# Kernel tuning notes

Measured on AMD Instinct MI355X. Metric: run time of the kernel, lower is better.

The kernel has to match this reference:

```python
import jax, jax.numpy as jnp
import numpy as np

N = 100000   # nodes
E = 1600000  # edges
G = 256      # graphs
NF = 7       # node features
EF = 3       # edge features (in/out)
UD = 2       # global feature dim
H = 128      # hidden dim
NL = 2       # MetaLayers = n_layers - 1
DOUT = 1


def _lin_init(k, fan_in, fan_out):
    return jax.random.normal(k, (fan_in, fan_out), jnp.float32) / np.sqrt(fan_in)


def _mlp2(h, W1, b1, W2, b2):
    return jax.nn.relu(h @ W1 + b1) @ W2 + b2


def setup_inputs() -> dict:
    key = jax.random.key(0)
    ks = jax.random.split(key, 40)
    x = jax.random.normal(ks[0], (N, NF), jnp.float32)
    edge_index = jax.random.randint(ks[1], (2, E), 0, N, jnp.int64)
    edge_attr = jax.random.normal(ks[2], (E, EF), jnp.float32)
    u = jax.random.normal(ks[3], (G, UD), jnp.float32)
    batch = jnp.sort(jax.random.randint(ks[4], (N,), 0, G, jnp.int64))
    # stacked per-layer params (NL identical layers)
    e_in = 2 * NF + EF          # 17
    n_in = NF + 3 * EF + UD     # 18
    eW1 = jnp.stack([_lin_init(ks[5 + i], e_in, H) for i in range(NL)])
    eb1 = jnp.zeros((NL, H), jnp.float32)
    eW2 = jnp.stack([_lin_init(ks[7 + i], H, EF) for i in range(NL)])
    eb2 = jnp.zeros((NL, EF), jnp.float32)
    nW1 = jnp.stack([_lin_init(ks[9 + i], n_in, H) for i in range(NL)])
    nb1 = jnp.zeros((NL, H), jnp.float32)
    nW2 = jnp.stack([_lin_init(ks[11 + i], H, NF) for i in range(NL)])
    nb2 = jnp.zeros((NL, NF), jnp.float32)
    # output head: 3*node_out + global_in -> H -> H -> H -> dim_out
    oW1 = _lin_init(ks[20], 3 * NF + UD, H); ob1 = jnp.zeros((H,), jnp.float32)
    oW2 = _lin_init(ks[21], H, H); ob2 = jnp.zeros((H,), jnp.float32)
    oW3 = _lin_init(ks[22], H, H); ob3 = jnp.zeros((H,), jnp.float32)
    oW4 = _lin_init(ks[23], H, DOUT); ob4 = jnp.zeros((DOUT,), jnp.float32)
    return dict(x=x, edge_attr=edge_attr, u=u,
                eW1=eW1, eb1=eb1, eW2=eW2, eb2=eb2,
                nW1=nW1, nb1=nb1, nW2=nW2, nb2=nb2,
                oW1=oW1, ob1=ob1, oW2=oW2, ob2=ob2,
                oW3=oW3, ob3=ob3, oW4=oW4, ob4=ob4,
                edge_index=edge_index, batch=batch)


def _segment_reduce3(vals, seg, num):
    # add / max (empty -> 0, matching torch_scatter fill) / mean
    s = jax.ops.segment_sum(vals, seg, num_segments=num)
    cnt = jax.ops.segment_sum(jnp.ones((vals.shape[0], 1), vals.dtype), seg, num_segments=num)
    m = jax.ops.segment_max(vals, seg, num_segments=num)
    m = jnp.where(cnt > 0, m, jnp.zeros_like(m))
    mean = s / jnp.maximum(cnt, 1.0)
    return s, m, mean, cnt


def reference(x, edge_attr, u, eW1, eb1, eW2, eb2, nW1, nb1, nW2, nb2,
              oW1, ob1, oW2, ob2, oW3, ob3, oW4, ob4, edge_index, batch):
    row, col = edge_index[0], edge_index[1]
    for l in range(NL):
        # EdgeModel: gather src/dest node feats + edge feats -> MLP
        e_in = jnp.concatenate([x[row], x[col], edge_attr], axis=1)  # [E, 2*NF+EF]
        edge_attr = _mlp2(e_in, eW1[l], eb1[l], eW2[l], eb2[l])      # [E, EF]
        # NodeModel: three scatter reductions over incoming edges (col)
        s, m, mean, _ = _segment_reduce3(edge_attr, col, N)
        n_in = jnp.concatenate([x, s, m, mean, u[batch]], axis=1)    # [N, NF+3*EF+UD]
        x = _mlp2(n_in, nW1[l], nb1[l], nW2[l], nb2[l])              # [N, NF]
    # global pools per graph
    s, m, mean, _ = _segment_reduce3(x, batch, G)
    h = jnp.concatenate([s, mean, m, u], axis=1)                     # [G, 3*NF+UD]
    h = jax.nn.relu(h @ oW1 + ob1)
    h = jax.nn.relu(h @ oW2 + ob2)
    h = jax.nn.relu(h @ oW3 + ob3)
    return h @ oW4 + ob4                                             # [G, DOUT]
```

## Files before the change

### kernel.cpp

```cpp
#include <hip/hip_runtime.h>

#define NN 100000
#define NE 1600000
#define NG 256
#define NB 391
#define NBH 1024
#define CHUNK 1563
#define NBINS 1024
#define NBUCK 782

typedef __attribute__((ext_vector_type(8))) short short8v;
typedef __attribute__((ext_vector_type(4))) float float4v;

__device__ __forceinline__ unsigned short f2bf(float f) {
    unsigned u = __float_as_uint(f);
    return (unsigned short)((u + 0x7FFFu + ((u >> 16) & 1u)) >> 16);
}
__device__ __forceinline__ unsigned fenc(float f) {
    unsigned u = __float_as_uint(f);
    return (u & 0x80000000u) ? ~u : (u | 0x80000000u);
}
__device__ __forceinline__ float fdec(unsigned e) {
    return __uint_as_float((e & 0x80000000u) ? (e & 0x7FFFFFFFu) : ~e);
}

__global__ __launch_bounds__(256) void hist_kernel(
    const int* __restrict__ col, unsigned* __restrict__ ghist) {
    __shared__ unsigned h[NBINS];
    int b = blockIdx.x;
    for (int i = threadIdx.x; i < NBINS; i += 256) h[i] = 0;
    __syncthreads();
    int e0 = b * CHUNK;
    int e1 = e0 + CHUNK; if (e1 > NE) e1 = NE;
    for (int e = e0 + threadIdx.x; e < e1; e += 256)
        atomicAdd(&h[col[e] >> 7], 1u);
    __syncthreads();
    for (int i = threadIdx.x; i < NBINS; i += 256)
        ghist[(size_t)b * NBINS + i] = h[i];
}

__global__ __launch_bounds__(1024) void scanB_kernel(
    const unsigned* __restrict__ ghist, unsigned* __restrict__ goff,
    unsigned* __restrict__ total) {
    __shared__ unsigned a[NBH], bb[NBH];
    int bin = blockIdx.x, t = threadIdx.x;
    unsigned v = ghist[(size_t)t * NBINS + bin];
    a[t] = v;
    __syncthreads();
    unsigned* src = a; unsigned* dst = bb;
    for (int off = 1; off < NBH; off <<= 1) {
        unsigned x = src[t];
        if (t >= off) x += src[t - off];
        dst[t] = x;
        __syncthreads();
        unsigned* tmp = src; src = dst; dst = tmp;
    }
    goff[(size_t)t * NBINS + bin] = src[t] - v;
    if (t == NBH - 1) total[bin] = src[t];
}

__global__ __launch_bounds__(1024) void scanC_kernel(
    const unsigned* __restrict__ total, unsigned* __restrict__ binbase) {
    __shared__ unsigned a[NBINS], bb[NBINS];
    int t = threadIdx.x;
    unsigned v = total[t];
    a[t] = v;
    __syncthreads();
    unsigned* src = a; unsigned* dst = bb;
    for (int off = 1; off < NBINS; off <<= 1) {
        unsigned x = src[t];
        if (t >= off) x += src[t - off];
        dst[t] = x;
        __syncthreads();
        unsigned* tmp = src; src = dst; dst = tmp;
    }
    binbase[t] = src[t] - v;
    if (t == NBINS - 1) binbase[NBINS] = src[t];
}

__global__ __launch_bounds__(256) void scatterD_kernel(
    const int* __restrict__ row, const int* __restrict__ col,
    const float* __restrict__ ea,
    const unsigned* __restrict__ goff, const unsigned* __restrict__ binbase,
    int2* __restrict__ rc, float* __restrict__ eab) {
    __shared__ unsigned cur[NBINS];
    int b = blockIdx.x;
    for (int i = threadIdx.x; i < NBINS; i += 256) cur[i] = 0;
    __syncthreads();
    int e0 = b * CHUNK;
    int e1 = e0 + CHUNK; if (e1 > NE) e1 = NE;
    const unsigned* grow = goff + (size_t)b * NBINS;
    for (int e = e0 + threadIdx.x; e < e1; e += 256) {
        int c = col[e];
        int bin = c >> 7;
        unsigned l = atomicAdd(&cur[bin], 1u);
        unsigned slot = binbase[bin] + grow[bin] + l;
        rc[slot] = make_int2(row[e], c);
        eab[(size_t)slot * 3 + 0] = ea[(size_t)e * 3 + 0];
        eab[(size_t)slot * 3 + 1] = ea[(size_t)e * 3 + 1];
        eab[(size_t)slot * 3 + 2] = ea[(size_t)e * 3 + 2];
    }
}

__global__ __launch_bounds__(256) void gbound_kernel(
    const int* __restrict__ batch, int* __restrict__ gstart) {
    int n = blockIdx.x * 256 + threadIdx.x;
    if (n >= NN) return;
    int b = batch[n];
    int bp = (n == 0) ? -1 : batch[n - 1];
    for (int g = bp + 1; g <= b; ++g) gstart[g] = n;
    if (n == NN - 1) {
        for (int g = b + 1; g <= NG; ++g) gstart[g] = NN;
    }
}

__global__ __launch_bounds__(256) void prep_kernel(
    const float* __restrict__ eW1, const float* __restrict__ eb1, const float* __restrict__ eW2,
    const float* __restrict__ nW1, const float* __restrict__ nb1, const float* __restrict__ nW2,
    short* __restrict__ ewf, float* __restrict__ w2f, float* __restrict__ b1f,
    float* __restrict__ nwt)
{
    int t = blockIdx.x * 256 + threadIdx.x;
    const int EWF = 2 * 4096;
    const int W2F = 2 * 1536;
    const int B1F = 2 * 512;
    const int NWT = 2 * 128 * 28;
    if (t < EWF) {
        int layer = t >> 12, r = t & 4095;
        int tt = r >> 9, r2 = r & 511;
        int l = r2 >> 3, i = r2 & 7;
        int kk = ((l >> 4) << 3) + i;
        int n = tt * 16 + (l & 15);
        float v = (kk < 17) ? eW1[layer * 17 * 128 + kk * 128 + n] : 0.f;
        ewf[t] = (short)f2bf(v);
    } else if (t < EWF + W2F) {
        int q = t - EWF;
        int layer = q / 1536, r = q % 1536;
        int l = r / 24, r2 = r % 24;
        int tt = r2 / 3, c = r2 % 3;
        int k = tt * 16 + (l & 15);
        w2f[q] = eW2[layer * 384 + k * 3 + c];
    } else if (t < EWF + W2F + B1F) {
        int q = t - EWF - W2F;
        int layer = q / 512, r = q % 512;
        int l = r / 8, tt = r % 8;
        b1f[q] = eb1[layer * 128 + tt * 16 + (l & 15)];
    } else if (t < EWF + W2F + B1F + NWT) {
        int q = t - EWF - W2F - B1F;
        int l = q / (128 * 28), rest = q % (128 * 28), j = rest / 28, i = rest % 28;
        float v = 0.f;
        if (i < 18)       v = nW1[l * 18 * 128 + i * 128 + j];
        else if (i == 18) v = nb1[l * 128 + j];
        else if (i < 26)  v = nW2[l * 128 * 7 + j * 7 + (i - 19)];
        nwt[q] = v;
    }
}

__global__ __launch_bounds__(256) void edge_kernel(
    const float* __restrict__ x, float* eab,
    const int2* __restrict__ rc,
    const short* __restrict__ ewf, const float* __restrict__ w2f,
    const float* __restrict__ b1f, const float* __restrict__ b2)
{
    int lane = threadIdx.x & 63;
    int l15 = lane & 15, lg = lane >> 4;
    int wid = (blockIdx.x * 256 + threadIdx.x) >> 6;
    int nwaves = gridDim.x * 4;

    short8v B1[8];
    #pragma unroll
    for (int t = 0; t < 8; ++t)
        B1[t] = *(const short8v*)(ewf + (t * 64 + lane) * 8);
    float w2a[8], w2b[8], w2c[8], b1v[8];
    #pragma unroll
    for (int t = 0; t < 8; ++t) {
        w2a[t] = w2f[lane * 24 + t * 3 + 0];
        w2b[t] = w2f[lane * 24 + t * 3 + 1];
        w2c[t] = w2f[lane * 24 + t * 3 + 2];
        b1v[t] = b1f[lane * 8 + t];
    }
    float bb0 = b2[0], bb1 = b2[1], bb2 = b2[2];

    const int NT = NE / 16;
    for (int tile = wid; tile < NT; tile += nwaves) {
        int s = tile * 16 + l15;
        int2 p = rc[s];
        const float* xr = x + (size_t)p.x * 7;
        const float* xc = x + (size_t)p.y * 7;
        const float* ep = eab + (size_t)s * 3;

        float av0 = 0.f, av1 = 0.f, av2 = 0.f, av3 = 0.f,
              av4 = 0.f, av5 = 0.f, av6 = 0.f, av7 = 0.f;
        if (lg == 0) {
            av0 = xr[0]; av1 = xr[1]; av2 = xr[2]; av3 = xr[3];
            av4 = xr[4]; av5 = xr[5]; av6 = xr[6]; av7 = xc[0];
        } else if (lg == 1) {
            av0 = xc[1]; av1 = xc[2]; av2 = xc[3]; av3 = xc[4];
            av4 = xc[5]; av5 = xc[6]; av6 = ep[0]; av7 = ep[1];
        } else if (lg == 2) {
            av0 = ep[2];
        }

        short8v A;
        A[0] = (short)f2bf(av0); A[1] = (short)f2bf(av1);
        A[2] = (short)f2bf(av2); A[3] = (short)f2bf(av3);
        A[4] = (short)f2bf(av4); A[5] = (short)f2bf(av5);
        A[6] = (short)f2bf(av6); A[7] = (short)f2bf(av7);

        float4v Z = {0.f, 0.f, 0.f, 0.f};
        float4v C[8];
        #pragma unroll
        for (int t = 0; t < 8; ++t)
            C[t] = __builtin_amdgcn_mfma_f32_16x16x32_bf16(A, B1[t], Z, 0, 0, 0);

        float p00 = 0.f, p01 = 0.f, p02 = 0.f;
        float p10 = 0.f, p11 = 0.f, p12 = 0.f;
        float p20 = 0.f, p21 = 0.f, p22 = 0.f;
        float p30 = 0.f, p31 = 0.f, p32 = 0.f;
        #pragma unroll
        for (int t = 0; t < 8; ++t) {
            float h0 = fmaxf(C[t][0] + b1v[t], 0.f);
            float h1 = fmaxf(C[t][1] + b1v[t], 0.f);
            float h2 = fmaxf(C[t][2] + b1v[t], 0.f);
            float h3 = fmaxf(C[t][3] + b1v[t], 0.f);
            p00 += h0 * w2a[t]; p01 += h0 * w2b[t]; p02 += h0 * w2c[t];
            p10 += h1 * w2a[t]; p11 += h1 * w2b[t]; p12 += h1 * w2c[t];
            p20 += h2 * w2a[t]; p21 += h2 * w2b[t]; p22 += h2 * w2c[t];
            p30 += h3 * w2a[t]; p31 += h3 * w2b[t]; p32 += h3 * w2c[t];
        }
        #pragma unroll
        for (int m = 1; m < 16; m <<= 1) {
            p00 += __shfl_xor(p00, m, 16); p01 += __shfl_xor(p01, m, 16); p02 += __shfl_xor(p02, m, 16);
            p10 += __shfl_xor(p10, m, 16); p11 += __shfl_xor(p11, m, 16); p12 += __shfl_xor(p12, m, 16);
            p20 += __shfl_xor(p20, m, 16); p21 += __shfl_xor(p21, m, 16); p22 += __shfl_xor(p22, m, 16);
            p30 += __shfl_xor(p30, m, 16); p31 += __shfl_xor(p31, m, 16); p32 += __shfl_xor(p32, m, 16);
        }
        if (l15 < 4) {
            float o0 = (l15 == 0) ? p00 : (l15 == 1) ? p10 : (l15 == 2) ? p20 : p30;
            float o1 = (l15 == 0) ? p01 : (l15 == 1) ? p11 : (l15 == 2) ? p21 : p31;
            float o2 = (l15 == 0) ? p02 : (l15 == 1) ? p12 : (l15 == 2) ? p22 : p32;
            size_t off = (size_t)(tile * 16 + lg * 4 + l15) * 3;
            eab[off + 0] = o0 + bb0;
            eab[off + 1] = o1 + bb1;
            eab[off + 2] = o2 + bb2;
        }
    }
}

__global__ __launch_bounds__(256) void bucket_reduce_kernel(
    const float* __restrict__ eab, const int2* __restrict__ rc,
    const unsigned* __restrict__ binbase,
    const float* __restrict__ u, const int* __restrict__ batch,
    float* __restrict__ nred)
{
    __shared__ float s0[128], s1[128], s2[128];
    __shared__ unsigned m0[128], m1[128], m2[128], cc[128];
    int bin = blockIdx.x, t = threadIdx.x;
    if (t < 128) {
        s0[t] = 0.f; s1[t] = 0.f; s2[t] = 0.f;
        m0[t] = 0u; m1[t] = 0u; m2[t] = 0u; cc[t] = 0u;
    }
    __syncthreads();
    unsigned beg = binbase[bin], end = binbase[bin + 1];
    for (unsigned k = beg + t; k < end; k += 256) {
        int c = rc[k].y & 127;
        float v0 = eab[(size_t)k * 3 + 0];
        float v1 = eab[(size_t)k * 3 + 1];
        float v2 = eab[(size_t)k * 3 + 2];
        atomicAdd(&s0[c], v0); atomicAdd(&s1[c], v1); atomicAdd(&s2[c], v2);
        atomicMax(&m0[c], fenc(v0)); atomicMax(&m1[c], fenc(v1)); atomicMax(&m2[c], fenc(v2));
        atomicAdd(&cc[c], 1u);
    }
    __syncthreads();
    if (t < 128) {
        int n = (bin << 7) + t;
        if (n < NN) {
            unsigned c = cc[t];
            float cf = (float)c;
            float inv = 1.f / fmaxf(cf, 1.f);
            float S0 = s0[t], S1 = s1[t], S2 = s2[t];
            float M0 = c ? fdec(m0[t]) : 0.f;
            float M1 = c ? fdec(m1[t]) : 0.f;
            float M2 = c ? fdec(m2[t]) : 0.f;
            int b = batch[n];
            float* o = nred + (size_t)n * 12;
            o[0] = S0; o[1] = S1; o[2] = S2;
            o[3] = M0; o[4] = M1; o[5] = M2;
            o[6] = S0 * inv; o[7] = S1 * inv; o[8] = S2 * inv;
            o[9] = u[b * 2 + 0]; o[10] = u[b * 2 + 1];
        }
    }
}

#define NMLP_BLOCKS 1024
#define NMLP_WAVES (NMLP_BLOCKS * 4)
__global__ __launch_bounds__(256, 4) void nodemlp_kernel(
    const float* x_in, const float* __restrict__ nred,
    const float* __restrict__ wt, const float* __restrict__ b2,
    float* x_out)
{
    int lane = threadIdx.x & 63;
    int wid = (blockIdx.x * 256 + threadIdx.x) >> 6;

    const float* ra = wt + lane * 28;
    const float* rb = wt + (lane + 64) * 28;
    float a0 = ra[0], a1 = ra[1], a2 = ra[2], a3 = ra[3], a4 = ra[4], a5 = ra[5],
          a6 = ra[6], a7 = ra[7], a8 = ra[8], a9 = ra[9], a10 = ra[10], a11 = ra[11],
          a12 = ra[12], a13 = ra[13], a14 = ra[14], a15 = ra[15], a16 = ra[16], a17 = ra[17],
          ab = ra[18], p0 = ra[19], p1 = ra[20], p2 = ra[21], p3 = ra[22], p4 = ra[23],
          p5 = ra[24], p6 = ra[25];
    float b0 = rb[0], b1 = rb[1], b2_ = rb[2], b3 = rb[3], b4 = rb[4], b5 = rb[5],
          b6 = rb[6], b7 = rb[7], b8 = rb[8], b9 = rb[9], b10 = rb[10], b11 = rb[11],
          b12 = rb[12], b13 = rb[13], b14 = rb[14], b15 = rb[15], b16 = rb[16], b17 = rb[17],
          bb = rb[18], q0 = rb[19], q1 = rb[20], q2 = rb[21], q3 = rb[22], q4 = rb[23],
          q5 = rb[24], q6 = rb[25];

    asm volatile("" : "+v"(a0), "+v"(a1), "+v"(a2), "+v"(a3), "+v"(a4), "+v"(a5),
                      "+v"(a6), "+v"(a7), "+v"(a8), "+v"(a9), "+v"(a10), "+v"(a11),
                      "+v"(a12), "+v"(a13), "+v"(a14), "+v"(a15), "+v"(a16), "+v"(a17),
                      "+v"(ab), "+v"(p0), "+v"(p1), "+v"(p2), "+v"(p3), "+v"(p4),
                      "+v"(p5), "+v"(p6));
    asm volatile("" : "+v"(b0), "+v"(b1), "+v"(b2_), "+v"(b3), "+v"(b4), "+v"(b5),
                      "+v"(b6), "+v"(b7), "+v"(b8), "+v"(b9), "+v"(b10), "+v"(b11),
                      "+v"(b12), "+v"(b13), "+v"(b14), "+v"(b15), "+v"(b16), "+v"(b17),
                      "+v"(bb), "+v"(q0), "+v"(q1), "+v"(q2), "+v"(q3), "+v"(q4),
                      "+v"(q5), "+v"(q6));

    float B0 = b2[0], B1 = b2[1], B2 = b2[2], B3 = b2[3], B4 = b2[4], B5 = b2[5], B6 = b2[6];

    const int nper = (NN + NMLP_WAVES - 1) / NMLP_WAVES;
    int n0 = wid * nper;
    int n1 = n0 + nper; if (n1 > NN) n1 = NN;

    #pragma unroll 2
    for (int n = n0; n < n1; ++n) {
        int nu = __builtin_amdgcn_readfirstlane(n);
        const float* xp = x_in + (size_t)nu * 7;
        const float* rp = nred + (size_t)nu * 12;
        float i0 = xp[0], i1 = xp[1], i2 = xp[2], i3 = xp[3], i4 = xp[4], i5 = xp[5], i6 = xp[6];
        float s0 = rp[0], s1 = rp[1], s2 = rp[2];
        float m0 = rp[3], m1 = rp[4], m2 = rp[5];
        float e0 = rp[6], e1 = rp[7], e2 = rp[8];
        float u0 = rp[9], u1 = rp[10];

        float ha = ab, hb = bb;
        ha += i0 * a0;  hb += i0 * b0;
        ha += i1 * a1;  hb += i1 * b1;
        ha += i2 * a2;  hb += i2 * b2_;
        ha += i3 * a3;  hb += i3 * b3;
        ha += i4 * a4;  hb += i4 * b4;
        ha += i5 * a5;  hb += i5 * b5;
        ha += i6 * a6;  hb += i6 * b6;
        ha += s0 * a7;  hb += s0 * b7;
        ha += s1 * a8;  hb += s1 * b8;
        ha += s2 * a9;  hb += s2 * b9;
        ha += m0 * a10; hb += m0 * b10;
        ha += m1 * a11; hb += m1 * b11;
        ha += m2 * a12; hb += m2 * b12;
        ha += e0 * a13; hb += e0 * b13;
        ha += e1 * a14; hb += e1 * b14;
        ha += e2 * a15; hb += e2 * b15;
        ha += u0 * a16; hb += u0 * b16;
        ha += u1 * a17; hb += u1 * b17;
        ha = fmaxf(ha, 0.f); hb = fmaxf(hb, 0.f);

        float c0 = ha * p0 + hb * q0;
        float c1 = ha * p1 + hb * q1;
        float c2 = ha * p2 + hb * q2;
        float c3 = ha * p3 + hb * q3;
        float c4 = ha * p4 + hb * q4;
        float c5 = ha * p5 + hb * q5;
        float c6 = ha * p6 + hb * q6;
        #pragma unroll
        for (int msk = 1; msk < 64; msk <<= 1) {
            c0 += __shfl_xor(c0, msk);
            c1 += __shfl_xor(c1, msk);
            c2 += __shfl_xor(c2, msk);
            c3 += __shfl_xor(c3, msk);
            c4 += __shfl_xor(c4, msk);
            c5 += __shfl_xor(c5, msk);
            c6 += __shfl_xor(c6, msk);
        }
        float o = c0 + B0;
        if (lane == 1) o = c1 + B1;
        if (lane == 2) o = c2 + B2;
        if (lane == 3) o = c3 + B3;
        if (lane == 4) o = c4 + B4;
        if (lane == 5) o = c5 + B5;
        if (lane == 6) o = c6 + B6;
        if (lane < 7) x_out[(size_t)nu * 7 + lane] = o;
    }
}

__global__ __launch_bounds__(256) void pool_head_kernel(
    const float* __restrict__ x, const int* __restrict__ gstart,
    const float* __restrict__ u,
    const float* __restrict__ oW1, const float* __restrict__ ob1,
    const float* __restrict__ oW2, const float* __restrict__ ob2,
    const float* __restrict__ oW3, const float* __restrict__ ob3,
    const float* __restrict__ oW4, const float* __restrict__ ob4,
    float* __restrict__ out)
{
    int g = blockIdx.x, tid = threadIdx.x;
    int lane = tid & 63, wv = tid >> 6;
    int gs = gstart[g], ge = gstart[g + 1];

    float s0 = 0.f, s1 = 0.f, s2 = 0.f, s3 = 0.f, s4 = 0.f, s5 = 0.f, s6 = 0.f;
    float m0 = -__builtin_inff(), m1 = m0, m2 = m0, m3 = m0, m4 = m0, m5 = m0, m6 = m0;
    for (int n = gs + tid; n < ge; n += 256) {
        const float* xp = x + (size_t)n * 7;
        float v0 = xp[0], v1 = xp[1], v2 = xp[2], v3 = xp[3], v4 = xp[4], v5 = xp[5], v6 = xp[6];
        s0 += v0; s1 += v1; s2 += v2; s3 += v3; s4 += v4; s5 += v5; s6 += v6;
        m0 = fmaxf(m0, v0); m1 = fmaxf(m1, v1); m2 = fmaxf(m2, v2); m3 = fmaxf(m3, v3);
        m4 = fmaxf(m4, v4); m5 = fmaxf(m5, v5); m6 = fmaxf(m6, v6);
    }
    #pragma unroll
    for (int msk = 1; msk < 64; msk <<= 1) {
        s0 += __shfl_xor(s0, msk); s1 += __shfl_xor(s1, msk); s2 += __shfl_xor(s2, msk);
        s3 += __shfl_xor(s3, msk); s4 += __shfl_xor(s4, msk); s5 += __shfl_xor(s5, msk);
        s6 += __shfl_xor(s6, msk);
        m0 = fmaxf(m0, __shfl_xor(m0, msk)); m1 = fmaxf(m1, __shfl_xor(m1, msk));
        m2 = fmaxf(m2, __shfl_xor(m2, msk)); m3 = fmaxf(m3, __shfl_xor(m3, msk));
        m4 = fmaxf(m4, __shfl_xor(m4, msk)); m5 = fmaxf(m5, __shfl_xor(m5, msk));
        m6 = fmaxf(m6, __shfl_xor(m6, msk));
    }
    __shared__ float red[4][14];
    __shared__ float hin[23];
    __shared__ float ha[128];
    __shared__ float hbuf[128];
    if (lane == 0) {
        red[wv][0] = s0; red[wv][1] = s1; red[wv][2] = s2; red[wv][3] = s3;
        red[wv][4] = s4; red[wv][5] = s5; red[wv][6] = s6;
        red[wv][7] = m0; red[wv][8] = m1; red[wv][9] = m2; red[wv][10] = m3;
        red[wv][11] = m4; red[wv][12] = m5; red[wv][13] = m6;
    }
    __syncthreads();
    if (tid < 7) {
        float S = red[0][tid] + red[1][tid] + red[2][tid] + red[3][tid];
        float M = fmaxf(fmaxf(red[0][7 + tid], red[1][7 + tid]),
                        fmaxf(red[2][7 + tid], red[3][7 + tid]));
        float cntf = (float)(ge - gs);
        if (ge == gs) M = 0.f;
        hin[tid] = S;
        hin[7 + tid] = S / fmaxf(cntf, 1.f);
        hin[14 + tid] = M;
    }
    if (tid < 2) hin[21 + tid] = u[g * 2 + tid];
    __syncthreads();

    float h = 0.f;
    if (tid < 128) {
        h = ob1[tid];
        for (int i = 0; i < 23; ++i) h += hin[i] * oW1[i * 128 + tid];
        ha[tid] = fmaxf(h, 0.f);
    }
    __syncthreads();
    if (tid < 128) {
        h = ob2[tid];
        for (int i = 0; i < 128; ++i) h += ha[i] * oW2[i * 128 + tid];
        hbuf[tid] = fmaxf(h, 0.f);
    }
    __syncthreads();
    if (tid < 128) {
        h = ob3[tid];
        for (int i = 0; i < 128; ++i) h += hbuf[i] * oW3[i * 128 + tid];
        ha[tid] = fmaxf(h, 0.f) * oW4[tid];
    }
    __syncthreads();
    if (tid == 0) {
        float acc = ob4[0];
        for (int i = 0; i < 128; ++i) acc += ha[i];
        out[g] = acc;
    }
}

extern "C" void kernel_launch(void* const* d_in, const int* in_sizes, int n_in,
                              void* d_out, int out_size, void* d_ws, size_t ws_size,
                              hipStream_t stream) {
    const float* x         = (const float*)d_in[0];
    const float* edge_attr = (const float*)d_in[1];
    const float* u         = (const float*)d_in[2];
    const float* eW1 = (const float*)d_in[3];
    const float* eb1 = (const float*)d_in[4];
    const float* eW2 = (const float*)d_in[5];
    const float* eb2 = (const float*)d_in[6];
    const float* nW1 = (const float*)d_in[7];
    const float* nb1 = (const float*)d_in[8];
    const float* nW2 = (const float*)d_in[9];
    const float* nb2 = (const float*)d_in[10];
    const float* oW1 = (const float*)d_in[11];
    const float* ob1 = (const float*)d_in[12];
    const float* oW2 = (const float*)d_in[13];
    const float* ob2 = (const float*)d_in[14];
    const float* oW3 = (const float*)d_in[15];
    const float* ob3 = (const float*)d_in[16];
    const float* oW4 = (const float*)d_in[17];
    const float* ob4 = (const float*)d_in[18];
    const int* edge_index = (const int*)d_in[19];
    const int* batch      = (const int*)d_in[20];
    const int* row = edge_index;
    const int* col = edge_index + NE;

    float* ws        = (float*)d_ws;
    float* eab       = ws;
    float* ws_x      = eab + (size_t)NE * 3;
    int2*  rc        = (int2*)(ws_x + (size_t)NN * 7);
    float* nred      = (float*)(rc + (size_t)NE);
    unsigned* ghist  = (unsigned*)(nred + (size_t)NN * 12);
    unsigned* goff   = ghist + (size_t)NBH * NBINS;
    unsigned* total  = goff + (size_t)NBH * NBINS;
    unsigned* binbase = total + NBINS;
    int* gstart      = (int*)(binbase + NBINS + 4);
    float* nwt       = (float*)(gstart + 260);
    float* w2f       = nwt + 2 * 128 * 28;
    float* b1f       = w2f + 2 * 1536;
    uintptr_t ewb    = ((uintptr_t)(b1f + 2 * 512) + 15) & ~(uintptr_t)15;
    short* ewf       = (short*)ewb;

    dim3 b256(256);
    dim3 gn(NB);

    hist_kernel<<<NBH, b256, 0, stream>>>(col, ghist);
    gbound_kernel<<<gn, b256, 0, stream>>>(batch, gstart);
    scanB_kernel<<<NBINS, 1024, 0, stream>>>(ghist, goff, total);
    scanC_kernel<<<1, 1024, 0, stream>>>(total, binbase);
    scatterD_kernel<<<NBH, b256, 0, stream>>>(row, col, edge_attr, goff, binbase, rc, eab);

    {
        int t = 2 * 4096 + 2 * 1536 + 2 * 512 + 2 * 128 * 28;
        prep_kernel<<<(t + 255) / 256, b256, 0, stream>>>(
            eW1, eb1, eW2, nW1, nb1, nW2, ewf, w2f, b1f, nwt);
    }

    dim3 gemf(2048);
    dim3 grb(NBUCK);

    edge_kernel<<<gemf, b256, 0, stream>>>(x, eab, rc, ewf, w2f, b1f, eb2);
    bucket_reduce_kernel<<<grb, b256, 0, stream>>>(eab, rc, binbase, u, batch, nred);
    nodemlp_kernel<<<NMLP_BLOCKS, b256, 0, stream>>>(x, nred, nwt, nb2, ws_x);

    edge_kernel<<<gemf, b256, 0, stream>>>(ws_x, eab, rc,
        ewf + 4096, w2f + 1536, b1f + 512, eb2 + 3);
    bucket_reduce_kernel<<<grb, b256, 0, stream>>>(eab, rc, binbase, u, batch, nred);
    nodemlp_kernel<<<NMLP_BLOCKS, b256, 0, stream>>>(ws_x, nred, nwt + 128 * 28, nb2 + 7, ws_x);

    pool_head_kernel<<<NG, b256, 0, stream>>>(ws_x, gstart, u,
        oW1, ob1, oW2, ob2, oW3, ob3, oW4, ob4, (float*)d_out);
}
```

Baseline: 417.7 us.

## Fuse edge MLP, bucket reduction and node MLP into one per-bin layer kernel

Replaces the three per-layer kernels (edge MLP, bucketed scatter reduce, node MLP) with one kernel launched per destination bin. Each block computes edge MLP outputs for the edges of its bin, reduces them straight into shared-memory sum/max/count accumulators, then runs the node MLP for the bin's 128 nodes. This removes the reload of edge outputs and the nred intermediate buffer round trip, and uses ping-pong x buffers. The trade-off is fewer blocks (782) with per-bin load imbalance, and the edge work is now limited to 4 waves per bin, which may lower parallelism compared with the 2048-block grid-stride edge kernel.

```diff
diff --git a/kernel.cpp b/kernel.cpp
--- a/kernel.cpp
+++ b/kernel.cpp
@@ -156,239 +156,209 @@
     }
 }
 
-__global__ __launch_bounds__(256) void edge_kernel(
-    const float* __restrict__ x, float* eab,
-    const int2* __restrict__ rc,
+__global__ __launch_bounds__(256) void fused_layer_kernel(
+    const float* __restrict__ x_in, float* eab,
+    const int2* __restrict__ rc, const unsigned* __restrict__ binbase,
     const short* __restrict__ ewf, const float* __restrict__ w2f,
-    const float* __restrict__ b1f, const float* __restrict__ b2)
+    const float* __restrict__ b1f, const float* __restrict__ b2e,
+    const float* __restrict__ nwt, const float* __restrict__ b2n,
+    const float* __restrict__ u, const int* __restrict__ batch,
+    float* __restrict__ x_out)
 {
-    int lane = threadIdx.x & 63;
+    __shared__ float ls0[128], ls1[128], ls2[128];
+    __shared__ unsigned lm0[128], lm1[128], lm2[128], lcc[128];
+    int tid = threadIdx.x, lane = tid & 63, wv = tid >> 6;
     int l15 = lane & 15, lg = lane >> 4;
-    int wid = (blockIdx.x * 256 + threadIdx.x) >> 6;
-    int nwaves = gridDim.x * 4;
-
-    short8v B1[8];
-    #pragma unroll
-    for (int t = 0; t < 8; ++t)
-        B1[t] = *(const short8v*)(ewf + (t * 64 + lane) * 8);
-    float w2a[8], w2b[8], w2c[8], b1v[8];
-    #pragma unroll
-    for (int t = 0; t < 8; ++t) {
-        w2a[t] = w2f[lane * 24 + t * 3 + 0];
-        w2b[t] = w2f[lane * 24 + t * 3 + 1];
-        w2c[t] = w2f[lane * 24 + t * 3 + 2];
-        b1v[t] = b1f[lane * 8 + t];
-    }
-    float bb0 = b2[0], bb1 = b2[1], bb2 = b2[2];
-
-    const int NT = NE / 16;
-    for (int tile = wid; tile < NT; tile += nwaves) {
-        int s = tile * 16 + l15;
-        int2 p = rc[s];
-        const float* xr = x + (size_t)p.x * 7;
-        const float* xc = x + (size_t)p.y * 7;
-        const float* ep = eab + (size_t)s * 3;
-
-        float av0 = 0.f, av1 = 0.f, av2 = 0.f, av3 = 0.f,
-              av4 = 0.f, av5 = 0.f, av6 = 0.f, av7 = 0.f;
-        if (lg == 0) {
-            av0 = xr[0]; av1 = xr[1]; av2 = xr[2]; av3 = xr[3];
-            av4 = xr[4]; av5 = xr[5]; av6 = xr[6]; av7 = xc[0];
-        } else if (lg == 1) {
-            av0 = xc[1]; av1 = xc[2]; av2 = xc[3]; av3 = xc[4];
-            av4 = xc[5]; av5 = xc[6]; av6 = ep[0]; av7 = ep[1];
-        } else if (lg == 2) {
-            av0 = ep[2];
-        }
-
-        short8v A;
-        A[0] = (short)f2bf(av0); A[1] = (short)f2bf(av1);
-        A[2] = (short)f2bf(av2); A[3] = (short)f2bf(av3);
-        A[4] = (short)f2bf(av4); A[5] = (short)f2bf(av5);
-        A[6] = (short)f2bf(av6); A[7] = (short)f2bf(av7);
-
-        float4v Z = {0.f, 0.f, 0.f, 0.f};
-        float4v C[8];
+    int bin = blockIdx.x;
+
+    if (tid < 128) {
+        ls0[tid] = 0.f; ls1[tid] = 0.f; ls2[tid] = 0.f;
+        lm0[tid] = 0u; lm1[tid] = 0u; lm2[tid] = 0u; lcc[tid] = 0u;
+    }
+    __syncthreads();
+
+    unsigned beg = binbase[bin], end = binbase[bin + 1];
+
+    {
+        short8v B1[8];
         #pragma unroll
         for (int t = 0; t < 8; ++t)
-            C[t] = __builtin_amdgcn_mfma_f32_16x16x32_bf16(A, B1[t], Z, 0, 0, 0);
-
-        float p00 = 0.f, p01 = 0.f, p02 = 0.f;
-        float p10 = 0.f, p11 = 0.f, p12 = 0.f;
-        float p20 = 0.f, p21 = 0.f, p22 = 0.f;
-        float p30 = 0.f, p31 = 0.f, p32 = 0.f;
+            B1[t] = *(const short8v*)(ewf + (t * 64 + lane) * 8);
+        float w2a[8], w2b[8], w2c[8], b1v[8];
         #pragma unroll
         for (int t = 0; t < 8; ++t) {
-            float h0 = fmaxf(C[t][0] + b1v[t], 0.f);
-            float h1 = fmaxf(C[t][1] + b1v[t], 0.f);
-            float h2 = fmaxf(C[t][2] + b1v[t], 0.f);
-            float h3 = fmaxf(C[t][3] + b1v[t], 0.f);
-            p00 += h0 * w2a[t]; p01 += h0 * w2b[t]; p02 += h0 * w2c[t];
-            p10 += h1 * w2a[t]; p11 += h1 * w2b[t]; p12 += h1 * w2c[t];
-            p20 += h2 * w2a[t]; p21 += h2 * w2b[t]; p22 += h2 * w2c[t];
-            p30 += h3 * w2a[t]; p31 += h3 * w2b[t]; p32 += h3 * w2c[t];
+            w2a[t] = w2f[lane * 24 + t * 3 + 0];
+            w2b[t] = w2f[lane * 24 + t * 3 + 1];
+            w2c[t] = w2f[lane * 24 + t * 3 + 2];
+            b1v[t] = b1f[lane * 8 + t];
         }
-        #pragma unroll
-        for (int m = 1; m < 16; m <<= 1) {
-            p00 += __shfl_xor(p00, m, 16); p01 += __shfl_xor(p01, m, 16); p02 += __shfl_xor(p02, m, 16);
-            p10 += __shfl_xor(p10, m, 16); p11 += __shfl_xor(p11, m, 16); p12 += __shfl_xor(p12, m, 16);
-            p20 += __shfl_xor(p20, m, 16); p21 += __shfl_xor(p21, m, 16); p22 += __shfl_xor(p22, m, 16);
-            p30 += __shfl_xor(p30, m, 16); p31 += __shfl_xor(p31, m, 16); p32 += __shfl_xor(p32, m, 16);
+        float bb0 = b2e[0], bb1 = b2e[1], bb2 = b2e[2];
+
+        int ntiles = (int)(end - beg + 15) >> 4;
+        for (int tb = wv; tb < ntiles; tb += 4) {
+            unsigned base = beg + (unsigned)tb * 16;
+            unsigned s = base + l15;
+            unsigned sc = (s < end) ? s : (end - 1);
+            int2 p = rc[sc];
+            const float* xr = x_in + (size_t)p.x * 7;
+            const float* xc = x_in + (size_t)p.y * 7;
+            const float* ep = eab + (size_t)sc * 3;
+
+            float av0 = 0.f, av1 = 0.f, av2 = 0.f, av3 = 0.f,
+                  av4 = 0.f, av5 = 0.f, av6 = 0.f, av7 = 0.f;
+            if (lg == 0) {
+                av0 = xr[0]; av1 = xr[1]; av2 = xr[2]; av3 = xr[3];
+                av4 = xr[4]; av5 = xr[5]; av6 = xr[6]; av7 = xc[0];
+            } else if (lg == 1) {
+                av0 = xc[1]; av1 = xc[2]; av2 = xc[3]; av3 = xc[4];
+                av4 = xc[5]; av5 = xc[6]; av6 = ep[0]; av7 = ep[1];
+            } else if (lg == 2) {
+                av0 = ep[2];
+            }
+
+            short8v A;
+            A[0] = (short)f2bf(av0); A[1] = (short)f2bf(av1);
+            A[2] = (short)f2bf(av2); A[3] = (short)f2bf(av3);
+            A[4] = (short)f2bf(av4); A[5] = (short)f2bf(av5);
+            A[6] = (short)f2bf(av6); A[7] = (short)f2bf(av7);
+
+            float4v Z = {0.f, 0.f, 0.f, 0.f};
+            float4v C[8];
+            #pragma unroll
+            for (int t = 0; t < 8; ++t)
+                C[t] = __builtin_amdgcn_mfma_f32_16x16x32_bf16(A, B1[t], Z, 0, 0, 0);
+
+            float p00 = 0.f, p01 = 0.f, p02 = 0.f;
+            float p10 = 0.f, p11 = 0.f, p12 = 0.f;
+            float p20 = 0.f, p21 = 0.f, p22 = 0.f;
+            float p30 = 0.f, p31 = 0.f, p32 = 0.f;
+            #pragma unroll
+            for (int t = 0; t < 8; ++t) {
+                float h0 = fmaxf(C[t][0] + b1v[t], 0.f);
+                float h1 = fmaxf(C[t][1] + b1v[t], 0.f);
+                float h2 = fmaxf(C[t][2] + b1v[t], 0.f);
+                float h3 = fmaxf(C[t][3] + b1v[t], 0.f);
+                p00 += h0 * w2a[t]; p01 += h0 * w2b[t]; p02 += h0 * w2c[t];
+                p10 += h1 * w2a[t]; p11 += h1 * w2b[t]; p12 += h1 * w2c[t];
+                p20 += h2 * w2a[t]; p21 += h2 * w2b[t]; p22 += h2 * w2c[t];
+                p30 += h3 * w2a[t]; p31 += h3 * w2b[t]; p32 += h3 * w2c[t];
+            }
+            #pragma unroll
+            for (int m = 1; m < 16; m <<= 1) {
+                p00 += __shfl_xor(p00, m, 16); p01 += __shfl_xor(p01, m, 16); p02 += __shfl_xor(p02, m, 16);
+                p10 += __shfl_xor(p10, m, 16); p11 += __shfl_xor(p11, m, 16); p12 += __shfl_xor(p12, m, 16);
+                p20 += __shfl_xor(p20, m, 16); p21 += __shfl_xor(p21, m, 16); p22 += __shfl_xor(p22, m, 16);
+                p30 += __shfl_xor(p30, m, 16); p31 += __shfl_xor(p31, m, 16); p32 += __shfl_xor(p32, m, 16);
+            }
+            int colo = __shfl(p.y, lg * 4 + (l15 & 3), 16);
+            if (l15 < 4) {
+                unsigned eo = base + (unsigned)(lg * 4 + l15);
+                if (eo < end) {
+                    float o0 = (l15 == 0) ? p00 : (l15 == 1) ? p10 : (l15 == 2) ? p20 : p30;
+                    float o1 = (l15 == 0) ? p01 : (l15 == 1) ? p11 : (l15 == 2) ? p21 : p31;
+                    float o2 = (l15 == 0) ? p02 : (l15 == 1) ? p12 : (l15 == 2) ? p22 : p32;
+                    o0 += bb0; o1 += bb1; o2 += bb2;
+                    size_t off = (size_t)eo * 3;
+                    eab[off + 0] = o0;
+                    eab[off + 1] = o1;
+                    eab[off + 2] = o2;
+                    int ln = colo & 127;
+                    atomicAdd(&ls0[ln], o0);
+                    atomicAdd(&ls1[ln], o1);
+                    atomicAdd(&ls2[ln], o2);
+                    atomicMax(&lm0[ln], fenc(o0));
+                    atomicMax(&lm1[ln], fenc(o1));
+                    atomicMax(&lm2[ln], fenc(o2));
+                    atomicAdd(&lcc[ln], 1u);
+                }
+            }
         }
-        if (l15 < 4) {
-            float o0 = (l15 == 0) ? p00 : (l15 == 1) ? p10 : (l15 == 2) ? p20 : p30;
-            float o1 = (l15 == 0) ? p01 : (l15 == 1) ? p11 : (l15 == 2) ? p21 : p31;
-            float o2 = (l15 == 0) ? p02 : (l15 == 1) ? p12 : (l15 == 2) ? p22 : p32;
-            size_t off = (size_t)(tile * 16 + lg * 4 + l15) * 3;
-            eab[off + 0] = o0 + bb0;
-            eab[off + 1] = o1 + bb1;
-            eab[off + 2] = o2 + bb2;
-        }
-    }
-}
-
-__global__ __launch_bounds__(256) void bucket_reduce_kernel(
-    const float* __restrict__ eab, const int2* __restrict__ rc,
-    const unsigned* __restrict__ binbase,
-    const float* __restrict__ u, const int* __restrict__ batch,
-    float* __restrict__ nred)
-{
-    __shared__ float s0[128], s1[128], s2[128];
-    __shared__ unsigned m0[128], m1[128], m2[128], cc[128];
-    int bin = blockIdx.x, t = threadIdx.x;
-    if (t < 128) {
-        s0[t] = 0.f; s1[t] = 0.f; s2[t] = 0.f;
-        m0[t] = 0u; m1[t] = 0u; m2[t] = 0u; cc[t] = 0u;
-    }
-    __syncthreads();
-    unsigned beg = binbase[bin], end = binbase[bin + 1];
-    for (unsigned k = beg + t; k < end; k += 256) {
-        int c = rc[k].y & 127;
-        float v0 = eab[(size_t)k * 3 + 0];
-        float v1 = eab[(size_t)k * 3 + 1];
-        float v2 = eab[(size_t)k * 3 + 2];
-        atomicAdd(&s0[c], v0); atomicAdd(&s1[c], v1); atomicAdd(&s2[c], v2);
-        atomicMax(&m0[c], fenc(v0)); atomicMax(&m1[c], fenc(v1)); atomicMax(&m2[c], fenc(v2));
-        atomicAdd(&cc[c], 1u);
-    }
-    __syncthreads();
-    if (t < 128) {
-        int n = (bin << 7) + t;
-        if (n < NN) {
-            unsigned c = cc[t];
+    }
+    __syncthreads();
+
+    {
+        const float* ra = nwt + lane * 28;
+        const float* rb = nwt + (lane + 64) * 28;
+        float a0 = ra[0], a1 = ra[1], a2 = ra[2], a3 = ra[3], a4 = ra[4], a5 = ra[5],
+              a6 = ra[6], a7 = ra[7], a8 = ra[8], a9 = ra[9], a10 = ra[10], a11 = ra[11],
+              a12 = ra[12], a13 = ra[13], a14 = ra[14], a15 = ra[15], a16 = ra[16], a17 = ra[17],
+              ab = ra[18], p0 = ra[19], p1 = ra[20], p2 = ra[21], p3 = ra[22], p4 = ra[23],
+              p5 = ra[24], p6 = ra[25];
+        float b0 = rb[0], b1 = rb[1], b2_ = rb[2], b3 = rb[3], b4 = rb[4], b5 = rb[5],
+              b6 = rb[6], b7 = rb[7], b8 = rb[8], b9 = rb[9], b10 = rb[10], b11 = rb[11],
+              b12 = rb[12], b13 = rb[13], b14 = rb[14], b15 = rb[15], b16 = rb[16], b17 = rb[17],
+              bb = rb[18], q0 = rb[19], q1 = rb[20], q2 = rb[21], q3 = rb[22], q4 = rb[23],
+              q5 = rb[24], q6 = rb[25];
+
+        float B0 = b2n[0], B1 = b2n[1], B2 = b2n[2], B3 = b2n[3],
+              B4 = b2n[4], B5 = b2n[5], B6 = b2n[6];
+
+        for (int i = 0; i < 32; ++i) {
+            int n = (bin << 7) + wv * 32 + i;
+            if (n >= NN) break;
+            int ln = wv * 32 + i;
+            int nu = __builtin_amdgcn_readfirstlane(n);
+            const float* xp = x_in + (size_t)nu * 7;
+            float i0 = xp[0], i1 = xp[1], i2 = xp[2], i3 = xp[3],
+                  i4 = xp[4], i5 = xp[5], i6 = xp[6];
+            float s0 = ls0[ln], s1 = ls1[ln], s2 = ls2[ln];
+            unsigned c = lcc[ln];
             float cf = (float)c;
             float inv = 1.f / fmaxf(cf, 1.f);
-            float S0 = s0[t], S1 = s1[t], S2 = s2[t];
-            float M0 = c ? fdec(m0[t]) : 0.f;
-            float M1 = c ? fdec(m1[t]) : 0.f;
-            float M2 = c ? fdec(m2[t]) : 0.f;
-            int b = batch[n];
-            float* o = nred + (size_t)n * 12;
-            o[0] = S0; o[1] = S1; o[2] = S2;
-            o[3] = M0; o[4] = M1; o[5] = M2;
-            o[6] = S0 * inv; o[7] = S1 * inv; o[8] = S2 * inv;
-            o[9] = u[b * 2 + 0]; o[10] = u[b * 2 + 1];
+            float m0 = c ? fdec(lm0[ln]) : 0.f;
+            float m1 = c ? fdec(lm1[ln]) : 0.f;
+            float m2 = c ? fdec(lm2[ln]) : 0.f;
+            float e0 = s0 * inv, e1 = s1 * inv, e2 = s2 * inv;
+            int b = batch[nu];
+            float u0 = u[b * 2 + 0], u1 = u[b * 2 + 1];
+
+            float ha = ab, hb = bb;
+            ha += i0 * a0;  hb += i0 * b0;
+            ha += i1 * a1;  hb += i1 * b1;
+            ha += i2 * a2;  hb += i2 * b2_;
+            ha += i3 * a3;  hb += i3 * b3;
+            ha += i4 * a4;  hb += i4 * b4;
+            ha += i5 * a5;  hb += i5 * b5;
+            ha += i6 * a6;  hb += i6 * b6;
+            ha += s0 * a7;  hb += s0 * b7;
+            ha += s1 * a8;  hb += s1 * b8;
+            ha += s2 * a9;  hb += s2 * b9;
+            ha += m0 * a10; hb += m0 * b10;
+            ha += m1 * a11; hb += m1 * b11;
+            ha += m2 * a12; hb += m2 * b12;
+            ha += e0 * a13; hb += e0 * b13;
+            ha += e1 * a14; hb += e1 * b14;
+            ha += e2 * a15; hb += e2 * b15;
+            ha += u0 * a16; hb += u0 * b16;
+            ha += u1 * a17; hb += u1 * b17;
+            ha = fmaxf(ha, 0.f); hb = fmaxf(hb, 0.f);
+
+            float c0 = ha * p0 + hb * q0;
+            float c1 = ha * p1 + hb * q1;
+            float c2 = ha * p2 + hb * q2;
+            float c3 = ha * p3 + hb * q3;
+            float c4 = ha * p4 + hb * q4;
+            float c5 = ha * p5 + hb * q5;
+            float c6 = ha * p6 + hb * q6;
+            #pragma unroll
+            for (int msk = 1; msk < 64; msk <<= 1) {
+                c0 += __shfl_xor(c0, msk);
+                c1 += __shfl_xor(c1, msk);
+                c2 += __shfl_xor(c2, msk);
+                c3 += __shfl_xor(c3, msk);
+                c4 += __shfl_xor(c4, msk);
+                c5 += __shfl_xor(c5, msk);
+                c6 += __shfl_xor(c6, msk);
+            }
+            float o = c0 + B0;
+            if (lane == 1) o = c1 + B1;
+            if (lane == 2) o = c2 + B2;
+            if (lane == 3) o = c3 + B3;
+            if (lane == 4) o = c4 + B4;
+            if (lane == 5) o = c5 + B5;
+            if (lane == 6) o = c6 + B6;
+            if (lane < 7) x_out[(size_t)nu * 7 + lane] = o;
         }
-    }
-}
-
-#define NMLP_BLOCKS 1024
-#define NMLP_WAVES (NMLP_BLOCKS * 4)
-__global__ __launch_bounds__(256, 4) void nodemlp_kernel(
-    const float* x_in, const float* __restrict__ nred,
-    const float* __restrict__ wt, const float* __restrict__ b2,
-    float* x_out)
-{
-    int lane = threadIdx.x & 63;
-    int wid = (blockIdx.x * 256 + threadIdx.x) >> 6;
-
-    const float* ra = wt + lane * 28;
-    const float* rb = wt + (lane + 64) * 28;
-    float a0 = ra[0], a1 = ra[1], a2 = ra[2], a3 = ra[3], a4 = ra[4], a5 = ra[5],
-          a6 = ra[6], a7 = ra[7], a8 = ra[8], a9 = ra[9], a10 = ra[10], a11 = ra[11],
-          a12 = ra[12], a13 = ra[13], a14 = ra[14], a15 = ra[15], a16 = ra[16], a17 = ra[17],
-          ab = ra[18], p0 = ra[19], p1 = ra[20], p2 = ra[21], p3 = ra[22], p4 = ra[23],
-          p5 = ra[24], p6 = ra[25];
-    float b0 = rb[0], b1 = rb[1], b2_ = rb[2], b3 = rb[3], b4 = rb[4], b5 = rb[5],
-          b6 = rb[6], b7 = rb[7], b8 = rb[8], b9 = rb[9], b10 = rb[10], b11 = rb[11],
-          b12 = rb[12], b13 = rb[13], b14 = rb[14], b15 = rb[15], b16 = rb[16], b17 = rb[17],
-          bb = rb[18], q0 = rb[19], q1 = rb[20], q2 = rb[21], q3 = rb[22], q4 = rb[23],
-          q5 = rb[24], q6 = rb[25];
-
-    asm volatile("" : "+v"(a0), "+v"(a1), "+v"(a2), "+v"(a3), "+v"(a4), "+v"(a5),
-                      "+v"(a6), "+v"(a7), "+v"(a8), "+v"(a9), "+v"(a10), "+v"(a11),
-                      "+v"(a12), "+v"(a13), "+v"(a14), "+v"(a15), "+v"(a16), "+v"(a17),
-                      "+v"(ab), "+v"(p0), "+v"(p1), "+v"(p2), "+v"(p3), "+v"(p4),
-                      "+v"(p5), "+v"(p6));
-    asm volatile("" : "+v"(b0), "+v"(b1), "+v"(b2_), "+v"(b3), "+v"(b4), "+v"(b5),
-                      "+v"(b6), "+v"(b7), "+v"(b8), "+v"(b9), "+v"(b10), "+v"(b11),
-                      "+v"(b12), "+v"(b13), "+v"(b14), "+v"(b15), "+v"(b16), "+v"(b17),
-                      "+v"(bb), "+v"(q0), "+v"(q1), "+v"(q2), "+v"(q3), "+v"(q4),
-                      "+v"(q5), "+v"(q6));
-
-    float B0 = b2[0], B1 = b2[1], B2 = b2[2], B3 = b2[3], B4 = b2[4], B5 = b2[5], B6 = b2[6];
-
-    const int nper = (NN + NMLP_WAVES - 1) / NMLP_WAVES;
-    int n0 = wid * nper;
-    int n1 = n0 + nper; if (n1 > NN) n1 = NN;
-
-    #pragma unroll 2
-    for (int n = n0; n < n1; ++n) {
-        int nu = __builtin_amdgcn_readfirstlane(n);
-        const float* xp = x_in + (size_t)nu * 7;
-        const float* rp = nred + (size_t)nu * 12;
-        float i0 = xp[0], i1 = xp[1], i2 = xp[2], i3 = xp[3], i4 = xp[4], i5 = xp[5], i6 = xp[6];
-        float s0 = rp[0], s1 = rp[1], s2 = rp[2];
-        float m0 = rp[3], m1 = rp[4], m2 = rp[5];
-        float e0 = rp[6], e1 = rp[7], e2 = rp[8];
-        float u0 = rp[9], u1 = rp[10];
-
-        float ha = ab, hb = bb;
-        ha += i0 * a0;  hb += i0 * b0;
-        ha += i1 * a1;  hb += i1 * b1;
-        ha += i2 * a2;  hb += i2 * b2_;
-        ha += i3 * a3;  hb += i3 * b3;
-        ha += i4 * a4;  hb += i4 * b4;
-        ha += i5 * a5;  hb += i5 * b5;
-        ha += i6 * a6;  hb += i6 * b6;
-        ha += s0 * a7;  hb += s0 * b7;
-        ha += s1 * a8;  hb += s1 * b8;
-        ha += s2 * a9;  hb += s2 * b9;
-        ha += m0 * a10; hb += m0 * b10;
-        ha += m1 * a11; hb += m1 * b11;
-        ha += m2 * a12; hb += m2 * b12;
-        ha += e0 * a13; hb += e0 * b13;
-        ha += e1 * a14; hb += e1 * b14;
-        ha += e2 * a15; hb += e2 * b15;
-        ha += u0 * a16; hb += u0 * b16;
-        ha += u1 * a17; hb += u1 * b17;
-        ha = fmaxf(ha, 0.f); hb = fmaxf(hb, 0.f);
-
-        float c0 = ha * p0 + hb * q0;
-        float c1 = ha * p1 + hb * q1;
-        float c2 = ha * p2 + hb * q2;
-        float c3 = ha * p3 + hb * q3;
-        float c4 = ha * p4 + hb * q4;
-        float c5 = ha * p5 + hb * q5;
-        float c6 = ha * p6 + hb * q6;
-        #pragma unroll
-        for (int msk = 1; msk < 64; msk <<= 1) {
-            c0 += __shfl_xor(c0, msk);
-            c1 += __shfl_xor(c1, msk);
-            c2 += __shfl_xor(c2, msk);
-            c3 += __shfl_xor(c3, msk);
-            c4 += __shfl_xor(c4, msk);
-            c5 += __shfl_xor(c5, msk);
-            c6 += __shfl_xor(c6, msk);
-        }
-        float o = c0 + B0;
-        if (lane == 1) o = c1 + B1;
-        if (lane == 2) o = c2 + B2;
-        if (lane == 3) o = c3 + B3;
-        if (lane == 4) o = c4 + B4;
-        if (lane == 5) o = c5 + B5;
-        if (lane == 6) o = c6 + B6;
-        if (lane < 7) x_out[(size_t)nu * 7 + lane] = o;
     }
 }
 
@@ -503,10 +473,10 @@
 
     float* ws        = (float*)d_ws;
     float* eab       = ws;
-    float* ws_x      = eab + (size_t)NE * 3;
-    int2*  rc        = (int2*)(ws_x + (size_t)NN * 7);
-    float* nred      = (float*)(rc + (size_t)NE);
-    unsigned* ghist  = (unsigned*)(nred + (size_t)NN * 12);
+    float* xA        = eab + (size_t)NE * 3;
+    float* xB        = xA + (size_t)NN * 7;
+    int2*  rc        = (int2*)(xB + (size_t)NN * 7);
+    unsigned* ghist  = (unsigned*)(rc + (size_t)NE);
     unsigned* goff   = ghist + (size_t)NBH * NBINS;
     unsigned* total  = goff + (size_t)NBH * NBINS;
     unsigned* binbase = total + NBINS;
@@ -532,18 +502,15 @@
             eW1, eb1, eW2, nW1, nb1, nW2, ewf, w2f, b1f, nwt);
     }
 
-    dim3 gemf(2048);
-    dim3 grb(NBUCK);
-
-    edge_kernel<<<gemf, b256, 0, stream>>>(x, eab, rc, ewf, w2f, b1f, eb2);
-    bucket_reduce_kernel<<<grb, b256, 0, stream>>>(eab, rc, binbase, u, batch, nred);
-    nodemlp_kernel<<<NMLP_BLOCKS, b256, 0, stream>>>(x, nred, nwt, nb2, ws_x);
-
-    edge_kernel<<<gemf, b256, 0, stream>>>(ws_x, eab, rc,
-        ewf + 4096, w2f + 1536, b1f + 512, eb2 + 3);
-    bucket_reduce_kernel<<<grb, b256, 0, stream>>>(eab, rc, binbase, u, batch, nred);
-    nodemlp_kernel<<<NMLP_BLOCKS, b256, 0, stream>>>(ws_x, nred, nwt + 128 * 28, nb2 + 7, ws_x);
-
-    pool_head_kernel<<<NG, b256, 0, stream>>>(ws_x, gstart, u,
+    dim3 gf(NBUCK);
+
+    fused_layer_kernel<<<gf, b256, 0, stream>>>(x, eab, rc, binbase,
+        ewf, w2f, b1f, eb2, nwt, nb2, u, batch, xA);
+
+    fused_layer_kernel<<<gf, b256, 0, stream>>>(xA, eab, rc, binbase,
+        ewf + 4096, w2f + 1536, b1f + 512, eb2 + 3,
+        nwt + 128 * 28, nb2 + 7, u, batch, xB);
+
+    pool_head_kernel<<<NG, b256, 0, stream>>>(xB, gstart, u,
         oW1, ob1, oW2, ob2, oW3, ob3, oW4, ob4, (float*)d_out);
 }
```

New measurement: 521.1 us. +24.8%, slower.

## Fully sort edges by destination node and replace atomic bucket reduce with segmented reduce

Applied to the files above, without the earlier changes.

Adds a second-level bucket sort that orders edges within each 128-node bin by exact destination node and records per-node CSR start offsets. The per-layer reduction then assigns 16 lanes per node to accumulate sum and max in registers with shuffle reductions, instead of LDS float atomics and encoded atomicMax. This removes atomic contention from the reduce step, which runs twice, at the cost of one extra sort pass over all edges plus temporary buffers for the intermediate edge order.

```diff
diff --git a/kernel.cpp b/kernel.cpp
--- a/kernel.cpp
+++ b/kernel.cpp
@@ -82,7 +82,7 @@
     const int* __restrict__ row, const int* __restrict__ col,
     const float* __restrict__ ea,
     const unsigned* __restrict__ goff, const unsigned* __restrict__ binbase,
-    int2* __restrict__ rc, float* __restrict__ eab) {
+    int2* __restrict__ rcT, float* __restrict__ eabT) {
     __shared__ unsigned cur[NBINS];
     int b = blockIdx.x;
     for (int i = threadIdx.x; i < NBINS; i += 256) cur[i] = 0;
@@ -95,10 +95,56 @@
         int bin = c >> 7;
         unsigned l = atomicAdd(&cur[bin], 1u);
         unsigned slot = binbase[bin] + grow[bin] + l;
-        rc[slot] = make_int2(row[e], c);
-        eab[(size_t)slot * 3 + 0] = ea[(size_t)e * 3 + 0];
-        eab[(size_t)slot * 3 + 1] = ea[(size_t)e * 3 + 1];
-        eab[(size_t)slot * 3 + 2] = ea[(size_t)e * 3 + 2];
+        rcT[slot] = make_int2(row[e], c);
+        eabT[(size_t)slot * 3 + 0] = ea[(size_t)e * 3 + 0];
+        eabT[(size_t)slot * 3 + 1] = ea[(size_t)e * 3 + 1];
+        eabT[(size_t)slot * 3 + 2] = ea[(size_t)e * 3 + 2];
+    }
+}
+
+__global__ __launch_bounds__(256) void bucketsort_kernel(
+    const int2* __restrict__ rcT, const float* __restrict__ eabT,
+    const unsigned* __restrict__ binbase,
+    int2* __restrict__ rc, float* __restrict__ eab, unsigned* __restrict__ start)
+{
+    __shared__ unsigned lcnt[128], sa[128], sb[128], lcur[128];
+    int bin = blockIdx.x, tid = threadIdx.x;
+    if (tid < 128) lcnt[tid] = 0;
+    __syncthreads();
+    unsigned beg = binbase[bin], end = binbase[bin + 1];
+    for (unsigned k = beg + tid; k < end; k += 256)
+        atomicAdd(&lcnt[rcT[k].y & 127], 1u);
+    __syncthreads();
+    if (tid < 128) sa[tid] = lcnt[tid];
+    __syncthreads();
+    unsigned* src = sa; unsigned* dst = sb;
+    for (int off = 1; off < 128; off <<= 1) {
+        if (tid < 128) {
+            unsigned v = src[tid];
+            if (tid >= off) v += src[tid - off];
+            dst[tid] = v;
+        }
+        __syncthreads();
+        unsigned* t2 = src; src = dst; dst = t2;
+    }
+    if (tid < 128) {
+        unsigned excl = src[tid] - lcnt[tid];
+        lcur[tid] = excl;
+        int n = (bin << 7) + tid;
+        if (n < NN) {
+            start[n] = beg + excl;
+            if (n == NN - 1) start[NN] = beg + excl + lcnt[tid];
+        }
+    }
+    __syncthreads();
+    for (unsigned k = beg + tid; k < end; k += 256) {
+        int2 p = rcT[k];
+        unsigned l = atomicAdd(&lcur[p.y & 127], 1u);
+        unsigned slot = beg + l;
+        rc[slot] = p;
+        eab[(size_t)slot * 3 + 0] = eabT[(size_t)k * 3 + 0];
+        eab[(size_t)slot * 3 + 1] = eabT[(size_t)k * 3 + 1];
+        eab[(size_t)slot * 3 + 2] = eabT[(size_t)k * 3 + 2];
     }
 }
 
@@ -247,48 +293,44 @@
     }
 }
 
-__global__ __launch_bounds__(256) void bucket_reduce_kernel(
-    const float* __restrict__ eab, const int2* __restrict__ rc,
-    const unsigned* __restrict__ binbase,
+__global__ __launch_bounds__(256) void reduce_kernel(
+    const float* __restrict__ eab, const unsigned* __restrict__ start,
     const float* __restrict__ u, const int* __restrict__ batch,
     float* __restrict__ nred)
 {
-    __shared__ float s0[128], s1[128], s2[128];
-    __shared__ unsigned m0[128], m1[128], m2[128], cc[128];
-    int bin = blockIdx.x, t = threadIdx.x;
-    if (t < 128) {
-        s0[t] = 0.f; s1[t] = 0.f; s2[t] = 0.f;
-        m0[t] = 0u; m1[t] = 0u; m2[t] = 0u; cc[t] = 0u;
-    }
-    __syncthreads();
-    unsigned beg = binbase[bin], end = binbase[bin + 1];
-    for (unsigned k = beg + t; k < end; k += 256) {
-        int c = rc[k].y & 127;
+    int gid = blockIdx.x * 256 + threadIdx.x;
+    int n = gid >> 4, sub = gid & 15;
+    if (n >= NN) return;
+    unsigned sbeg = start[n], send = start[n + 1];
+
+    float s0 = 0.f, s1 = 0.f, s2 = 0.f;
+    float m0 = -__builtin_inff(), m1 = -__builtin_inff(), m2 = -__builtin_inff();
+    for (unsigned k = sbeg + sub; k < send; k += 16) {
         float v0 = eab[(size_t)k * 3 + 0];
         float v1 = eab[(size_t)k * 3 + 1];
         float v2 = eab[(size_t)k * 3 + 2];
-        atomicAdd(&s0[c], v0); atomicAdd(&s1[c], v1); atomicAdd(&s2[c], v2);
-        atomicMax(&m0[c], fenc(v0)); atomicMax(&m1[c], fenc(v1)); atomicMax(&m2[c], fenc(v2));
-        atomicAdd(&cc[c], 1u);
-    }
-    __syncthreads();
-    if (t < 128) {
-        int n = (bin << 7) + t;
-        if (n < NN) {
-            unsigned c = cc[t];
-            float cf = (float)c;
-            float inv = 1.f / fmaxf(cf, 1.f);
-            float S0 = s0[t], S1 = s1[t], S2 = s2[t];
-            float M0 = c ? fdec(m0[t]) : 0.f;
-            float M1 = c ? fdec(m1[t]) : 0.f;
-            float M2 = c ? fdec(m2[t]) : 0.f;
-            int b = batch[n];
-            float* o = nred + (size_t)n * 12;
-            o[0] = S0; o[1] = S1; o[2] = S2;
-            o[3] = M0; o[4] = M1; o[5] = M2;
-            o[6] = S0 * inv; o[7] = S1 * inv; o[8] = S2 * inv;
-            o[9] = u[b * 2 + 0]; o[10] = u[b * 2 + 1];
-        }
+        s0 += v0; s1 += v1; s2 += v2;
+        m0 = fmaxf(m0, v0); m1 = fmaxf(m1, v1); m2 = fmaxf(m2, v2);
+    }
+    #pragma unroll
+    for (int msk = 1; msk < 16; msk <<= 1) {
+        s0 += __shfl_xor(s0, msk, 16);
+        s1 += __shfl_xor(s1, msk, 16);
+        s2 += __shfl_xor(s2, msk, 16);
+        m0 = fmaxf(m0, __shfl_xor(m0, msk, 16));
+        m1 = fmaxf(m1, __shfl_xor(m1, msk, 16));
+        m2 = fmaxf(m2, __shfl_xor(m2, msk, 16));
+    }
+    if (sub == 0) {
+        float deg = (float)(send - sbeg);
+        if (send == sbeg) { m0 = 0.f; m1 = 0.f; m2 = 0.f; }
+        float inv = 1.f / fmaxf(deg, 1.f);
+        int b = batch[n];
+        float* o = nred + (size_t)n * 12;
+        o[0] = s0; o[1] = s1; o[2] = s2;
+        o[3] = m0; o[4] = m1; o[5] = m2;
+        o[6] = s0 * inv; o[7] = s1 * inv; o[8] = s2 * inv;
+        o[9] = u[b * 2 + 0]; o[10] = u[b * 2 + 1];
     }
 }
 
@@ -503,14 +545,17 @@
 
     float* ws        = (float*)d_ws;
     float* eab       = ws;
-    float* ws_x      = eab + (size_t)NE * 3;
+    float* eabT      = eab + (size_t)NE * 3;
+    float* ws_x      = eabT + (size_t)NE * 3;
     int2*  rc        = (int2*)(ws_x + (size_t)NN * 7);
-    float* nred      = (float*)(rc + (size_t)NE);
+    int2*  rcT       = rc + (size_t)NE;
+    float* nred      = (float*)(rcT + (size_t)NE);
     unsigned* ghist  = (unsigned*)(nred + (size_t)NN * 12);
     unsigned* goff   = ghist + (size_t)NBH * NBINS;
     unsigned* total  = goff + (size_t)NBH * NBINS;
     unsigned* binbase = total + NBINS;
-    int* gstart      = (int*)(binbase + NBINS + 4);
+    unsigned* startv = binbase + NBINS + 4;
+    int* gstart      = (int*)(startv + NN + 4);
     float* nwt       = (float*)(gstart + 260);
     float* w2f       = nwt + 2 * 128 * 28;
     float* b1f       = w2f + 2 * 1536;
@@ -524,7 +569,8 @@
     gbound_kernel<<<gn, b256, 0, stream>>>(batch, gstart);
     scanB_kernel<<<NBINS, 1024, 0, stream>>>(ghist, goff, total);
     scanC_kernel<<<1, 1024, 0, stream>>>(total, binbase);
-    scatterD_kernel<<<NBH, b256, 0, stream>>>(row, col, edge_attr, goff, binbase, rc, eab);
+    scatterD_kernel<<<NBH, b256, 0, stream>>>(row, col, edge_attr, goff, binbase, rcT, eabT);
+    bucketsort_kernel<<<NBUCK, b256, 0, stream>>>(rcT, eabT, binbase, rc, eab, startv);
 
     {
         int t = 2 * 4096 + 2 * 1536 + 2 * 512 + 2 * 128 * 28;
@@ -533,15 +579,15 @@
     }
 
     dim3 gemf(2048);
-    dim3 grb(NBUCK);
+    dim3 gr((NN * 16 + 255) / 256);
 
     edge_kernel<<<gemf, b256, 0, stream>>>(x, eab, rc, ewf, w2f, b1f, eb2);
-    bucket_reduce_kernel<<<grb, b256, 0, stream>>>(eab, rc, binbase, u, batch, nred);
+    reduce_kernel<<<gr, b256, 0, stream>>>(eab, startv, u, batch, nred);
     nodemlp_kernel<<<NMLP_BLOCKS, b256, 0, stream>>>(x, nred, nwt, nb2, ws_x);
 
     edge_kernel<<<gemf, b256, 0, stream>>>(ws_x, eab, rc,
         ewf + 4096, w2f + 1536, b1f + 512, eb2 + 3);
-    bucket_reduce_kernel<<<grb, b256, 0, stream>>>(eab, rc, binbase, u, batch, nred);
+    reduce_kernel<<<gr, b256, 0, stream>>>(eab, startv, u, batch, nred);
     nodemlp_kernel<<<NMLP_BLOCKS, b256, 0, stream>>>(ws_x, nred, nwt + 128 * 28, nb2 + 7, ws_x);
 
     pool_head_kernel<<<NG, b256, 0, stream>>>(ws_x, gstart, u,
```

Result: faster. 400.0 us (-4.2%).
